# Kernel tuning notes

Measured on AMD Instinct MI355X. Metric: run time of the kernel, lower is better.

## Reference

```python
import jax, jax.numpy as jnp
import numpy as np

WINDOW = 128
LOOK_BACKWARD = 1
LOOK_FORWARD = 0  # causal=True -> look_forward defaults to 0
THETA = 10000.0


def look_around(x, backward=LOOK_BACKWARD, forward=LOOK_FORWARD, pad_value=-1):
    # x: (b, w, n, ...). Pad along window axis, concat shifted slices along token axis.
    w = x.shape[1]
    pad_width = [(0, 0)] * x.ndim
    pad_width[1] = (backward, forward)
    padded = jnp.pad(x, pad_width, constant_values=pad_value)
    return jnp.concatenate([padded[:, i:i + w] for i in range(forward + backward + 1)], axis=2)


def rotate_half(x):
    x1, x2 = jnp.split(x, 2, axis=-1)
    return jnp.concatenate((-x2, x1), axis=-1)


def setup_inputs() -> dict:
    key = jax.random.key(0)
    kq, kk, kv = jax.random.split(key, 3)
    shape = (32, 4096, 64)
    return {
        "q": jax.random.normal(kq, shape, dtype=jnp.float32),
        "k": jax.random.normal(kk, shape, dtype=jnp.float32),
        "v": jax.random.normal(kv, shape, dtype=jnp.float32),
    }


def reference(q, k, v):
    b, n, d = q.shape
    scale = d ** -0.5
    w = n // WINDOW

    bq = q.reshape(b, w, WINDOW, d) * scale
    bk = look_around(k.reshape(b, w, WINDOW, d), pad_value=-1.0)
    bv = look_around(v.reshape(b, w, WINDOW, d), pad_value=-1.0)
    j = bk.shape[2]  # (1 + look_backward + look_forward) * WINDOW = 256

    # rotary pos emb (SinusoidalEmbeddings, no xpos -> scale = 1)
    inv_freq = 1.0 / (THETA ** (jnp.arange(0, d, 2, dtype=jnp.float32) / d))
    t = jnp.arange(j, dtype=jnp.float32)
    freqs = jnp.einsum('i,j->ij', t, inv_freq)
    freqs = jnp.concatenate((freqs, freqs), axis=-1)  # (j, d)
    q_freqs = freqs[-WINDOW:]  # queries align to the last WINDOW positions
    bq = bq * jnp.cos(q_freqs) + rotate_half(bq) * jnp.sin(q_freqs)
    bk = bk * jnp.cos(freqs) + rotate_half(bk) * jnp.sin(freqs)

    # position bookkeeping for masks
    seq = jnp.arange(n)
    b_t = seq.reshape(1, w, WINDOW)           # (1, w, i)
    bq_t = b_t[..., :, None]                  # (1, w, i, 1)
    bq_k = look_around(b_t, pad_value=-1)[..., None, :]  # (1, w, 1, j)
    pad_mask = bq_k == -1
    causal_mask = bq_t < bq_k

    sim = jnp.einsum('bwie,bwje->bwij', bq, bk)  # (b, w, i, j)
    mask_value = -jnp.finfo(sim.dtype).max
    sim = jnp.where(causal_mask | pad_mask, mask_value, sim)

    attn = jax.nn.softmax(sim, axis=-1)
    out = jnp.einsum('bwij,bwje->bwie', attn, bv)
    return out.reshape(b, n, d)
```

## Files before the change

kernel.cpp:

```cpp
#include <hip/hip_runtime.h>
#include <hip/hip_bf16.h>

#define BDIM 512

typedef __attribute__((ext_vector_type(8))) _Float16 f16x8;
typedef __attribute__((ext_vector_type(4))) _Float16 f16x4;
typedef __attribute__((ext_vector_type(4))) float f32x4;

__global__ __launch_bounds__(512, 4)
void la_kernel(const float* __restrict__ qg, const float* __restrict__ kg,
               const float* __restrict__ vg, float* __restrict__ outg)
{
    __shared__ _Float16 Ks[128][72];
    __shared__ _Float16 Vt[64][140];

    const int ww = blockIdx.x, bb = blockIdx.y;
    const int tid = threadIdx.x;
    const size_t qbase = ((size_t)bb * 4096 + (size_t)ww * 128) * 64;
    const int srow0 = ww * 128 - 128;
    const float NEG = -3.0e38f;
    const float NLT32 = -0.28782313662425572f;

    const int wv = tid >> 6, lane = tid & 63, g = lane >> 4, c = lane & 15;
    const int qrow = wv * 16 + c;

    f16x8 qa0, qa1;
    {
        const float* p = qg + qbase + (size_t)qrow * 64 + 8 * g;
        float4 a0 = *(const float4*)p;
        float4 a1 = *(const float4*)(p + 4);
        float4 b0 = *(const float4*)(p + 32);
        float4 b1 = *(const float4*)(p + 36);
        float ra[8] = {a0.x,a0.y,a0.z,a0.w,a1.x,a1.y,a1.z,a1.w};
        float rb[8] = {b0.x,b0.y,b0.z,b0.w,b1.x,b1.y,b1.z,b1.w};
        float tq = (float)(128 + qrow);
        #pragma unroll
        for (int u = 0; u < 8; ++u) {
            float invf = __expf((float)(8 * g + u) * NLT32);
            float sn, cs; __sincosf(tq * invf, &sn, &cs);
            float a = ra[u] * 0.125f, b = rb[u] * 0.125f;
            qa0[u] = (_Float16)(a * cs - b * sn);
            qa1[u] = (_Float16)(b * cs + a * sn);
        }
    }

    f32x4 accO[4];
    #pragma unroll
    for (int nt = 0; nt < 4; ++nt) accO[nt] = (f32x4){0.f,0.f,0.f,0.f};
    float m = NEG, s = 0.f;

    #pragma unroll 1
    for (int h = 0; h < 2; ++h) {
        if (h == 0 && ww == 0) continue;
        if (h == 1) __syncthreads();

        #pragma unroll
        for (int it = 0; it < 2; ++it) {
            int task = tid + it * 512;
            int j = task >> 3, cb = (task & 7) << 2;
            int tj = 128 * h + j;
            const float* p = kg + ((size_t)bb * 4096 + srow0 + tj) * 64 + cb;
            float4 x1 = *(const float4*)p;
            float4 x2 = *(const float4*)(p + 32);
            const float* x1p = &x1.x;
            const float* x2p = &x2.x;
            f16x4 lo, hi;
            #pragma unroll
            for (int u = 0; u < 4; ++u) {
                float invf = __expf((float)(cb + u) * NLT32);
                float sn, cs; __sincosf((float)tj * invf, &sn, &cs);
                lo[u] = (_Float16)(x1p[u] * cs - x2p[u] * sn);
                hi[u] = (_Float16)(x2p[u] * cs + x1p[u] * sn);
            }
            *(f16x4*)&Ks[j][cb]      = lo;
            *(f16x4*)&Ks[j][cb + 32] = hi;
        }

        {
            int jq = tid >> 4, eq = tid & 15;
            int colb = ((jq & 24) << 2) + 8 * (jq & 3) + 4 * ((jq >> 2) & 1);
            float4 x[4];
            #pragma unroll
            for (int w = 0; w < 4; ++w)
                x[w] = *(const float4*)(vg + ((size_t)bb * 4096 + srow0 + 128 * h + 4 * jq + w) * 64 + 4 * eq);
            #pragma unroll
            for (int u = 0; u < 4; ++u) {
                f16x4 o;
                o[0] = (_Float16)((const float*)&x[0])[u];
                o[1] = (_Float16)((const float*)&x[1])[u];
                o[2] = (_Float16)((const float*)&x[2])[u];
                o[3] = (_Float16)((const float*)&x[3])[u];
                *(f16x4*)&Vt[4 * eq + u][colb] = o;
            }
        }

        __syncthreads();

        #pragma unroll
        for (int ch = 0; ch < 2; ++ch) {
            f32x4 acc[4];
            #pragma unroll
            for (int jt = 0; jt < 4; ++jt) acc[jt] = (f32x4){0.f,0.f,0.f,0.f};

            #pragma unroll
            for (int jt = 0; jt < 4; ++jt) {
                int row = ch * 64 + jt * 16 + c;
                f16x8 kb0 = *(const f16x8*)&Ks[row][8 * g];
                f16x8 kb1 = *(const f16x8*)&Ks[row][32 + 8 * g];
                acc[jt] = __builtin_amdgcn_mfma_f32_16x16x32_f16(kb0, qa0, acc[jt], 0, 0, 0);
                acc[jt] = __builtin_amdgcn_mfma_f32_16x16x32_f16(kb1, qa1, acc[jt], 0, 0, 0);
            }

            if (h == 1) {
                #pragma unroll
                for (int jt = 0; jt < 4; ++jt)
                    #pragma unroll
                    for (int r = 0; r < 4; ++r) {
                        int jj = ch * 64 + jt * 16 + 4 * g + r;
                        if (jj > qrow) acc[jt][r] = NEG;
                    }
            }

            float mx = NEG;
            #pragma unroll
            for (int jt = 0; jt < 4; ++jt)
                #pragma unroll
                for (int r = 0; r < 4; ++r) mx = fmaxf(mx, acc[jt][r]);
            mx = fmaxf(mx, __shfl_xor(mx, 16));
            mx = fmaxf(mx, __shfl_xor(mx, 32));

            float mnew = fmaxf(m, mx);
            float alpha = __expf(m - mnew);

            float ps = 0.f;
            f16x8 pa[2];
            #pragma unroll
            for (int jt = 0; jt < 4; ++jt)
                #pragma unroll
                for (int r = 0; r < 4; ++r) {
                    float p = __expf(acc[jt][r] - mnew);
                    ps += p;
                    pa[jt >> 1][(jt & 1) * 4 + r] = (_Float16)p;
                }
            ps += __shfl_xor(ps, 16);
            ps += __shfl_xor(ps, 32);

            s = s * alpha + ps;
            m = mnew;

            float alphaD[4];
            #pragma unroll
            for (int r = 0; r < 4; ++r)
                alphaD[r] = __shfl(alpha, (lane & 48) | (4 * g + r));
            #pragma unroll
            for (int nt = 0; nt < 4; ++nt)
                #pragma unroll
                for (int r = 0; r < 4; ++r) accO[nt][r] *= alphaD[r];

            #pragma unroll
            for (int st = 0; st < 2; ++st) {
                #pragma unroll
                for (int nt = 0; nt < 4; ++nt) {
                    f16x8 vb = *(const f16x8*)&Vt[nt * 16 + c][ch * 64 + st * 32 + 8 * g];
                    accO[nt] = __builtin_amdgcn_mfma_f32_16x16x32_f16(pa[st], vb, accO[nt], 0, 0, 0);
                }
            }
        }
    }

    float rcp = 1.0f / s;
    float rcpD[4];
    #pragma unroll
    for (int r = 0; r < 4; ++r)
        rcpD[r] = __shfl(rcp, (lane & 48) | (4 * g + r));

    float* op = outg + qbase + (size_t)(wv * 16) * 64;
    #pragma unroll
    for (int nt = 0; nt < 4; ++nt)
        #pragma unroll
        for (int r = 0; r < 4; ++r)
            op[(size_t)(4 * g + r) * 64 + nt * 16 + c] = accO[nt][r] * rcpD[r];
}

extern "C" void kernel_launch(void* const* d_in, const int* in_sizes, int n_in,
                              void* d_out, int out_size, void* d_ws, size_t ws_size,
                              hipStream_t stream) {
    (void)in_sizes; (void)n_in; (void)out_size; (void)d_ws; (void)ws_size;
    const float* q = (const float*)d_in[0];
    const float* k = (const float*)d_in[1];
    const float* v = (const float*)d_in[2];
    float* out = (float*)d_out;
    dim3 grid(32, 32);
    la_kernel<<<grid, BDIM, 0, stream>>>(q, k, v, out);
}
```

Before: 37.47 us.

## Process two windows per block, reusing shared K/V tile across windows

Each block now handles two adjacent query windows and keeps a two-slot shared buffer for K/V blocks, so the middle key/value block is loaded, rotary-encoded and converted once instead of twice. Rotary inverse frequencies are also precomputed once per thread rather than per element. This cuts global K/V traffic and rotary math by about a quarter. The cost is twice the shared memory, half as many blocks (fewer waves to hide latency), and serialized window processing inside a block.

```diff
diff --git a/kernel.cpp b/kernel.cpp
--- a/kernel.cpp
+++ b/kernel.cpp
@@ -11,55 +11,34 @@
 void la_kernel(const float* __restrict__ qg, const float* __restrict__ kg,
                const float* __restrict__ vg, float* __restrict__ outg)
 {
-    __shared__ _Float16 Ks[128][72];
-    __shared__ _Float16 Vt[64][140];
-
-    const int ww = blockIdx.x, bb = blockIdx.y;
+    __shared__ _Float16 Ks[2][128][72];
+    __shared__ _Float16 Vt[2][64][140];
+
+    const int wp = blockIdx.x, bb = blockIdx.y;
     const int tid = threadIdx.x;
-    const size_t qbase = ((size_t)bb * 4096 + (size_t)ww * 128) * 64;
-    const int srow0 = ww * 128 - 128;
+    const int wv = tid >> 6, lane = tid & 63, g = lane >> 4, c = lane & 15;
+    const int base = 256 * wp - 128;
     const float NEG = -3.0e38f;
     const float NLT32 = -0.28782313662425572f;
 
-    const int wv = tid >> 6, lane = tid & 63, g = lane >> 4, c = lane & 15;
-    const int qrow = wv * 16 + c;
-
-    f16x8 qa0, qa1;
-    {
-        const float* p = qg + qbase + (size_t)qrow * 64 + 8 * g;
-        float4 a0 = *(const float4*)p;
-        float4 a1 = *(const float4*)(p + 4);
-        float4 b0 = *(const float4*)(p + 32);
-        float4 b1 = *(const float4*)(p + 36);
-        float ra[8] = {a0.x,a0.y,a0.z,a0.w,a1.x,a1.y,a1.z,a1.w};
-        float rb[8] = {b0.x,b0.y,b0.z,b0.w,b1.x,b1.y,b1.z,b1.w};
-        float tq = (float)(128 + qrow);
-        #pragma unroll
-        for (int u = 0; u < 8; ++u) {
-            float invf = __expf((float)(8 * g + u) * NLT32);
-            float sn, cs; __sincosf(tq * invf, &sn, &cs);
-            float a = ra[u] * 0.125f, b = rb[u] * 0.125f;
-            qa0[u] = (_Float16)(a * cs - b * sn);
-            qa1[u] = (_Float16)(b * cs + a * sn);
-        }
-    }
-
-    f32x4 accO[4];
+    const int cbK = (tid & 7) << 2;
+    float invfK[4];
     #pragma unroll
-    for (int nt = 0; nt < 4; ++nt) accO[nt] = (f32x4){0.f,0.f,0.f,0.f};
-    float m = NEG, s = 0.f;
-
-    #pragma unroll 1
-    for (int h = 0; h < 2; ++h) {
-        if (h == 0 && ww == 0) continue;
-        if (h == 1) __syncthreads();
-
+    for (int u = 0; u < 4; ++u) invfK[u] = __expf((float)(cbK + u) * NLT32);
+    float invfQ[8];
+    #pragma unroll
+    for (int u = 0; u < 8; ++u) invfQ[u] = __expf((float)(8 * g + u) * NLT32);
+
+    const int jqV = tid >> 4, eqV = tid & 15;
+    const int colbV = ((jqV & 24) << 2) + 8 * (jqV & 3) + 4 * ((jqV >> 2) & 1);
+
+    auto stage = [&](int mm) {
+        int sl = mm & 1;
         #pragma unroll
         for (int it = 0; it < 2; ++it) {
-            int task = tid + it * 512;
-            int j = task >> 3, cb = (task & 7) << 2;
-            int tj = 128 * h + j;
-            const float* p = kg + ((size_t)bb * 4096 + srow0 + tj) * 64 + cb;
+            int j = (tid + it * 512) >> 3;
+            int t = 128 * mm + j;
+            const float* p = kg + ((size_t)bb * 4096 + base + t) * 64 + cbK;
             float4 x1 = *(const float4*)p;
             float4 x2 = *(const float4*)(p + 32);
             const float* x1p = &x1.x;
@@ -67,119 +46,155 @@
             f16x4 lo, hi;
             #pragma unroll
             for (int u = 0; u < 4; ++u) {
-                float invf = __expf((float)(cb + u) * NLT32);
-                float sn, cs; __sincosf((float)tj * invf, &sn, &cs);
+                float sn, cs; __sincosf((float)t * invfK[u], &sn, &cs);
                 lo[u] = (_Float16)(x1p[u] * cs - x2p[u] * sn);
                 hi[u] = (_Float16)(x2p[u] * cs + x1p[u] * sn);
             }
-            *(f16x4*)&Ks[j][cb]      = lo;
-            *(f16x4*)&Ks[j][cb + 32] = hi;
-        }
-
+            *(f16x4*)&Ks[sl][j][cbK]      = lo;
+            *(f16x4*)&Ks[sl][j][cbK + 32] = hi;
+        }
+        float4 x[4];
+        #pragma unroll
+        for (int w = 0; w < 4; ++w)
+            x[w] = *(const float4*)(vg + ((size_t)bb * 4096 + base + 128 * mm + 4 * jqV + w) * 64 + 4 * eqV);
+        #pragma unroll
+        for (int u = 0; u < 4; ++u) {
+            f16x4 o;
+            o[0] = (_Float16)((const float*)&x[0])[u];
+            o[1] = (_Float16)((const float*)&x[1])[u];
+            o[2] = (_Float16)((const float*)&x[2])[u];
+            o[3] = (_Float16)((const float*)&x[3])[u];
+            *(f16x4*)&Vt[sl][4 * eqV + u][colbV] = o;
+        }
+    };
+
+    auto computeWin = [&](int wi) {
+        const int qrow = tid < 0 ? 0 : (wv * 16 + c);
+        const int tq = 128 * (wi + 1) + qrow;
+
+        f16x8 qa0, qa1;
         {
-            int jq = tid >> 4, eq = tid & 15;
-            int colb = ((jq & 24) << 2) + 8 * (jq & 3) + 4 * ((jq >> 2) & 1);
-            float4 x[4];
-            #pragma unroll
-            for (int w = 0; w < 4; ++w)
-                x[w] = *(const float4*)(vg + ((size_t)bb * 4096 + srow0 + 128 * h + 4 * jq + w) * 64 + 4 * eq);
-            #pragma unroll
-            for (int u = 0; u < 4; ++u) {
-                f16x4 o;
-                o[0] = (_Float16)((const float*)&x[0])[u];
-                o[1] = (_Float16)((const float*)&x[1])[u];
-                o[2] = (_Float16)((const float*)&x[2])[u];
-                o[3] = (_Float16)((const float*)&x[3])[u];
-                *(f16x4*)&Vt[4 * eq + u][colb] = o;
+            const float* p = qg + ((size_t)bb * 4096 + base + tq) * 64 + 8 * g;
+            float4 a0 = *(const float4*)p;
+            float4 a1 = *(const float4*)(p + 4);
+            float4 b0 = *(const float4*)(p + 32);
+            float4 b1 = *(const float4*)(p + 36);
+            float ra[8] = {a0.x,a0.y,a0.z,a0.w,a1.x,a1.y,a1.z,a1.w};
+            float rb[8] = {b0.x,b0.y,b0.z,b0.w,b1.x,b1.y,b1.z,b1.w};
+            #pragma unroll
+            for (int u = 0; u < 8; ++u) {
+                float sn, cs; __sincosf((float)tq * invfQ[u], &sn, &cs);
+                float a = ra[u] * 0.125f, b = rb[u] * 0.125f;
+                qa0[u] = (_Float16)(a * cs - b * sn);
+                qa1[u] = (_Float16)(b * cs + a * sn);
             }
         }
 
-        __syncthreads();
-
-        #pragma unroll
-        for (int ch = 0; ch < 2; ++ch) {
-            f32x4 acc[4];
-            #pragma unroll
-            for (int jt = 0; jt < 4; ++jt) acc[jt] = (f32x4){0.f,0.f,0.f,0.f};
-
-            #pragma unroll
-            for (int jt = 0; jt < 4; ++jt) {
-                int row = ch * 64 + jt * 16 + c;
-                f16x8 kb0 = *(const f16x8*)&Ks[row][8 * g];
-                f16x8 kb1 = *(const f16x8*)&Ks[row][32 + 8 * g];
-                acc[jt] = __builtin_amdgcn_mfma_f32_16x16x32_f16(kb0, qa0, acc[jt], 0, 0, 0);
-                acc[jt] = __builtin_amdgcn_mfma_f32_16x16x32_f16(kb1, qa1, acc[jt], 0, 0, 0);
-            }
-
-            if (h == 1) {
+        f32x4 accO[4];
+        #pragma unroll
+        for (int nt = 0; nt < 4; ++nt) accO[nt] = (f32x4){0.f,0.f,0.f,0.f};
+        float m = NEG, s = 0.f;
+
+        #pragma unroll 1
+        for (int mm = wi; mm <= wi + 1; ++mm) {
+            if (wp == 0 && mm == 0) continue;
+            const int sl = mm & 1;
+            const bool causal = (mm == wi + 1);
+
+            #pragma unroll
+            for (int ch = 0; ch < 2; ++ch) {
+                f32x4 acc[4];
+                #pragma unroll
+                for (int jt = 0; jt < 4; ++jt) acc[jt] = (f32x4){0.f,0.f,0.f,0.f};
+
+                #pragma unroll
+                for (int jt = 0; jt < 4; ++jt) {
+                    int row = ch * 64 + jt * 16 + c;
+                    f16x8 kb0 = *(const f16x8*)&Ks[sl][row][8 * g];
+                    f16x8 kb1 = *(const f16x8*)&Ks[sl][row][32 + 8 * g];
+                    acc[jt] = __builtin_amdgcn_mfma_f32_16x16x32_f16(kb0, qa0, acc[jt], 0, 0, 0);
+                    acc[jt] = __builtin_amdgcn_mfma_f32_16x16x32_f16(kb1, qa1, acc[jt], 0, 0, 0);
+                }
+
+                if (causal) {
+                    #pragma unroll
+                    for (int jt = 0; jt < 4; ++jt)
+                        #pragma unroll
+                        for (int r = 0; r < 4; ++r) {
+                            int jj = ch * 64 + jt * 16 + 4 * g + r;
+                            if (jj > qrow) acc[jt][r] = NEG;
+                        }
+                }
+
+                float mx = NEG;
                 #pragma unroll
                 for (int jt = 0; jt < 4; ++jt)
                     #pragma unroll
+                    for (int r = 0; r < 4; ++r) mx = fmaxf(mx, acc[jt][r]);
+                mx = fmaxf(mx, __shfl_xor(mx, 16));
+                mx = fmaxf(mx, __shfl_xor(mx, 32));
+
+                float mnew = fmaxf(m, mx);
+                float alpha = __expf(m - mnew);
+
+                float ps = 0.f;
+                f16x8 pa[2];
+                #pragma unroll
+                for (int jt = 0; jt < 4; ++jt)
+                    #pragma unroll
                     for (int r = 0; r < 4; ++r) {
-                        int jj = ch * 64 + jt * 16 + 4 * g + r;
-                        if (jj > qrow) acc[jt][r] = NEG;
+                        float p = __expf(acc[jt][r] - mnew);
+                        ps += p;
+                        pa[jt >> 1][(jt & 1) * 4 + r] = (_Float16)p;
                     }
-            }
-
-            float mx = NEG;
-            #pragma unroll
-            for (int jt = 0; jt < 4; ++jt)
-                #pragma unroll
-                for (int r = 0; r < 4; ++r) mx = fmaxf(mx, acc[jt][r]);
-            mx = fmaxf(mx, __shfl_xor(mx, 16));
-            mx = fmaxf(mx, __shfl_xor(mx, 32));
-
-            float mnew = fmaxf(m, mx);
-            float alpha = __expf(m - mnew);
-
-            float ps = 0.f;
-            f16x8 pa[2];
-            #pragma unroll
-            for (int jt = 0; jt < 4; ++jt)
-                #pragma unroll
-                for (int r = 0; r < 4; ++r) {
-                    float p = __expf(acc[jt][r] - mnew);
-                    ps += p;
-                    pa[jt >> 1][(jt & 1) * 4 + r] = (_Float16)p;
-                }
-            ps += __shfl_xor(ps, 16);
-            ps += __shfl_xor(ps, 32);
-
-            s = s * alpha + ps;
-            m = mnew;
-
-            float alphaD[4];
-            #pragma unroll
-            for (int r = 0; r < 4; ++r)
-                alphaD[r] = __shfl(alpha, (lane & 48) | (4 * g + r));
-            #pragma unroll
-            for (int nt = 0; nt < 4; ++nt)
-                #pragma unroll
-                for (int r = 0; r < 4; ++r) accO[nt][r] *= alphaD[r];
-
-            #pragma unroll
-            for (int st = 0; st < 2; ++st) {
-                #pragma unroll
-                for (int nt = 0; nt < 4; ++nt) {
-                    f16x8 vb = *(const f16x8*)&Vt[nt * 16 + c][ch * 64 + st * 32 + 8 * g];
-                    accO[nt] = __builtin_amdgcn_mfma_f32_16x16x32_f16(pa[st], vb, accO[nt], 0, 0, 0);
+                ps += __shfl_xor(ps, 16);
+                ps += __shfl_xor(ps, 32);
+
+                s = s * alpha + ps;
+                m = mnew;
+
+                float alphaD[4];
+                #pragma unroll
+                for (int r = 0; r < 4; ++r)
+                    alphaD[r] = __shfl(alpha, (lane & 48) | (4 * g + r));
+                #pragma unroll
+                for (int nt = 0; nt < 4; ++nt)
+                    #pragma unroll
+                    for (int r = 0; r < 4; ++r) accO[nt][r] *= alphaD[r];
+
+                #pragma unroll
+                for (int st = 0; st < 2; ++st) {
+                    #pragma unroll
+                    for (int nt = 0; nt < 4; ++nt) {
+                        f16x8 vb = *(const f16x8*)&Vt[sl][nt * 16 + c][ch * 64 + st * 32 + 8 * g];
+                        accO[nt] = __builtin_amdgcn_mfma_f32_16x16x32_f16(pa[st], vb, accO[nt], 0, 0, 0);
+                    }
                 }
             }
         }
-    }
-
-    float rcp = 1.0f / s;
-    float rcpD[4];
-    #pragma unroll
-    for (int r = 0; r < 4; ++r)
-        rcpD[r] = __shfl(rcp, (lane & 48) | (4 * g + r));
-
-    float* op = outg + qbase + (size_t)(wv * 16) * 64;
-    #pragma unroll
-    for (int nt = 0; nt < 4; ++nt)
+
+        float rcp = 1.0f / s;
+        float rcpD[4];
         #pragma unroll
         for (int r = 0; r < 4; ++r)
-            op[(size_t)(4 * g + r) * 64 + nt * 16 + c] = accO[nt][r] * rcpD[r];
+            rcpD[r] = __shfl(rcp, (lane & 48) | (4 * g + r));
+
+        float* op = outg + ((size_t)bb * 4096 + base + 128 * (wi + 1) + wv * 16) * 64;
+        #pragma unroll
+        for (int nt = 0; nt < 4; ++nt)
+            #pragma unroll
+            for (int r = 0; r < 4; ++r)
+                op[(size_t)(4 * g + r) * 64 + nt * 16 + c] = accO[nt][r] * rcpD[r];
+    };
+
+    if (wp > 0) stage(0);
+    stage(1);
+    __syncthreads();
+    computeWin(0);
+    __syncthreads();
+    stage(2);
+    __syncthreads();
+    computeWin(1);
 }
 
 extern "C" void kernel_launch(void* const* d_in, const int* in_sizes, int n_in,
@@ -190,6 +205,6 @@
     const float* k = (const float*)d_in[1];
     const float* v = (const float*)d_in[2];
     float* out = (float*)d_out;
-    dim3 grid(32, 32);
+    dim3 grid(16, 32);
     la_kernel<<<grid, BDIM, 0, stream>>>(q, k, v, out);
 }
```

Result: faster. 34.00 us (-9.3%).

## Halve block size, give each wave two query tiles, skip fully masked chunks

Applied to the files above, without the earlier changes.

The block shrinks from 8 to 4 waves, and each wave now processes two 16-row query tiles, so every K/V fragment read from LDS feeds twice as many MFMAs. Inverse frequencies are hoisted out of the rotary loops. For the diagonal window, key chunks that are entirely above the causal diagonal for a query tile are skipped. The trade-off is higher register pressure from doubled accumulators and fewer threads to load and rotate K/V into shared memory.

```diff
diff --git a/kernel.cpp b/kernel.cpp
--- a/kernel.cpp
+++ b/kernel.cpp
@@ -1,13 +1,13 @@
 #include <hip/hip_runtime.h>
 #include <hip/hip_bf16.h>
 
-#define BDIM 512
+#define BDIM 256
 
 typedef __attribute__((ext_vector_type(8))) _Float16 f16x8;
 typedef __attribute__((ext_vector_type(4))) _Float16 f16x4;
 typedef __attribute__((ext_vector_type(4))) float f32x4;
 
-__global__ __launch_bounds__(512, 4)
+__global__ __launch_bounds__(256, 4)
 void la_kernel(const float* __restrict__ qg, const float* __restrict__ kg,
                const float* __restrict__ vg, float* __restrict__ outg)
 {
@@ -16,50 +16,60 @@
 
     const int ww = blockIdx.x, bb = blockIdx.y;
     const int tid = threadIdx.x;
-    const size_t qbase = ((size_t)bb * 4096 + (size_t)ww * 128) * 64;
+    const int wv = tid >> 6, lane = tid & 63, g = lane >> 4, c = lane & 15;
+    const size_t rowb = (size_t)bb * 4096;
     const int srow0 = ww * 128 - 128;
     const float NEG = -3.0e38f;
     const float NLT32 = -0.28782313662425572f;
 
-    const int wv = tid >> 6, lane = tid & 63, g = lane >> 4, c = lane & 15;
-    const int qrow = wv * 16 + c;
-
-    f16x8 qa0, qa1;
+    const int cbK = (tid & 7) << 2;
+    float invfK[4];
+    #pragma unroll
+    for (int u = 0; u < 4; ++u) invfK[u] = __expf((float)(cbK + u) * NLT32);
+
+    f16x8 qa0[2], qa1[2];
     {
-        const float* p = qg + qbase + (size_t)qrow * 64 + 8 * g;
-        float4 a0 = *(const float4*)p;
-        float4 a1 = *(const float4*)(p + 4);
-        float4 b0 = *(const float4*)(p + 32);
-        float4 b1 = *(const float4*)(p + 36);
-        float ra[8] = {a0.x,a0.y,a0.z,a0.w,a1.x,a1.y,a1.z,a1.w};
-        float rb[8] = {b0.x,b0.y,b0.z,b0.w,b1.x,b1.y,b1.z,b1.w};
-        float tq = (float)(128 + qrow);
-        #pragma unroll
-        for (int u = 0; u < 8; ++u) {
-            float invf = __expf((float)(8 * g + u) * NLT32);
-            float sn, cs; __sincosf(tq * invf, &sn, &cs);
-            float a = ra[u] * 0.125f, b = rb[u] * 0.125f;
-            qa0[u] = (_Float16)(a * cs - b * sn);
-            qa1[u] = (_Float16)(b * cs + a * sn);
+        float invfQ[8];
+        #pragma unroll
+        for (int u = 0; u < 8; ++u) invfQ[u] = __expf((float)(8 * g + u) * NLT32);
+        #pragma unroll
+        for (int mt = 0; mt < 2; ++mt) {
+            const int qrow = wv * 32 + mt * 16 + c;
+            const float* p = qg + (rowb + ww * 128 + qrow) * 64 + 8 * g;
+            float4 a0 = *(const float4*)p;
+            float4 a1 = *(const float4*)(p + 4);
+            float4 b0 = *(const float4*)(p + 32);
+            float4 b1 = *(const float4*)(p + 36);
+            float ra[8] = {a0.x,a0.y,a0.z,a0.w,a1.x,a1.y,a1.z,a1.w};
+            float rb[8] = {b0.x,b0.y,b0.z,b0.w,b1.x,b1.y,b1.z,b1.w};
+            float tq = (float)(128 + qrow);
+            #pragma unroll
+            for (int u = 0; u < 8; ++u) {
+                float sn, cs; __sincosf(tq * invfQ[u], &sn, &cs);
+                float a = ra[u] * 0.125f, b = rb[u] * 0.125f;
+                qa0[mt][u] = (_Float16)(a * cs - b * sn);
+                qa1[mt][u] = (_Float16)(b * cs + a * sn);
+            }
         }
     }
 
-    f32x4 accO[4];
+    f32x4 accO[2][4];
     #pragma unroll
-    for (int nt = 0; nt < 4; ++nt) accO[nt] = (f32x4){0.f,0.f,0.f,0.f};
-    float m = NEG, s = 0.f;
+    for (int mt = 0; mt < 2; ++mt)
+        #pragma unroll
+        for (int nt = 0; nt < 4; ++nt) accO[mt][nt] = (f32x4){0.f,0.f,0.f,0.f};
+    float m[2] = {NEG, NEG}, s[2] = {0.f, 0.f};
 
     #pragma unroll 1
     for (int h = 0; h < 2; ++h) {
         if (h == 0 && ww == 0) continue;
-        if (h == 1) __syncthreads();
-
-        #pragma unroll
-        for (int it = 0; it < 2; ++it) {
-            int task = tid + it * 512;
-            int j = task >> 3, cb = (task & 7) << 2;
-            int tj = 128 * h + j;
-            const float* p = kg + ((size_t)bb * 4096 + srow0 + tj) * 64 + cb;
+        if (h == 1 && ww != 0) __syncthreads();
+
+        #pragma unroll
+        for (int it = 0; it < 4; ++it) {
+            int j = (tid + it * 256) >> 3;
+            int t = 128 * h + j;
+            const float* p = kg + (rowb + srow0 + t) * 64 + cbK;
             float4 x1 = *(const float4*)p;
             float4 x2 = *(const float4*)(p + 32);
             const float* x1p = &x1.x;
@@ -67,22 +77,23 @@
             f16x4 lo, hi;
             #pragma unroll
             for (int u = 0; u < 4; ++u) {
-                float invf = __expf((float)(cb + u) * NLT32);
-                float sn, cs; __sincosf((float)tj * invf, &sn, &cs);
+                float sn, cs; __sincosf((float)t * invfK[u], &sn, &cs);
                 lo[u] = (_Float16)(x1p[u] * cs - x2p[u] * sn);
                 hi[u] = (_Float16)(x2p[u] * cs + x1p[u] * sn);
             }
-            *(f16x4*)&Ks[j][cb]      = lo;
-            *(f16x4*)&Ks[j][cb + 32] = hi;
-        }
-
-        {
-            int jq = tid >> 4, eq = tid & 15;
+            *(f16x4*)&Ks[j][cbK]      = lo;
+            *(f16x4*)&Ks[j][cbK + 32] = hi;
+        }
+
+        #pragma unroll
+        for (int it = 0; it < 2; ++it) {
+            int task = tid + it * 256;
+            int jq = task >> 4, eq = task & 15;
             int colb = ((jq & 24) << 2) + 8 * (jq & 3) + 4 * ((jq >> 2) & 1);
             float4 x[4];
             #pragma unroll
             for (int w = 0; w < 4; ++w)
-                x[w] = *(const float4*)(vg + ((size_t)bb * 4096 + srow0 + 128 * h + 4 * jq + w) * 64 + 4 * eq);
+                x[w] = *(const float4*)(vg + (rowb + srow0 + 128 * h + 4 * jq + w) * 64 + 4 * eq);
             #pragma unroll
             for (int u = 0; u < 4; ++u) {
                 f16x4 o;
@@ -97,89 +108,98 @@
         __syncthreads();
 
         #pragma unroll
-        for (int ch = 0; ch < 2; ++ch) {
-            f32x4 acc[4];
-            #pragma unroll
-            for (int jt = 0; jt < 4; ++jt) acc[jt] = (f32x4){0.f,0.f,0.f,0.f};
-
-            #pragma unroll
-            for (int jt = 0; jt < 4; ++jt) {
-                int row = ch * 64 + jt * 16 + c;
-                f16x8 kb0 = *(const f16x8*)&Ks[row][8 * g];
-                f16x8 kb1 = *(const f16x8*)&Ks[row][32 + 8 * g];
-                acc[jt] = __builtin_amdgcn_mfma_f32_16x16x32_f16(kb0, qa0, acc[jt], 0, 0, 0);
-                acc[jt] = __builtin_amdgcn_mfma_f32_16x16x32_f16(kb1, qa1, acc[jt], 0, 0, 0);
-            }
-
-            if (h == 1) {
+        for (int mt = 0; mt < 2; ++mt) {
+            const int qrow = wv * 32 + mt * 16 + c;
+            #pragma unroll
+            for (int ch = 0; ch < 2; ++ch) {
+                if (h == 1 && ch == 1 && (wv * 32 + mt * 16) <= 48) continue;
+
+                f32x4 acc[4];
+                #pragma unroll
+                for (int jt = 0; jt < 4; ++jt) acc[jt] = (f32x4){0.f,0.f,0.f,0.f};
+
+                #pragma unroll
+                for (int jt = 0; jt < 4; ++jt) {
+                    int row = ch * 64 + jt * 16 + c;
+                    f16x8 kb0 = *(const f16x8*)&Ks[row][8 * g];
+                    f16x8 kb1 = *(const f16x8*)&Ks[row][32 + 8 * g];
+                    acc[jt] = __builtin_amdgcn_mfma_f32_16x16x32_f16(kb0, qa0[mt], acc[jt], 0, 0, 0);
+                    acc[jt] = __builtin_amdgcn_mfma_f32_16x16x32_f16(kb1, qa1[mt], acc[jt], 0, 0, 0);
+                }
+
+                if (h == 1) {
+                    #pragma unroll
+                    for (int jt = 0; jt < 4; ++jt)
+                        #pragma unroll
+                        for (int r = 0; r < 4; ++r) {
+                            int jj = ch * 64 + jt * 16 + 4 * g + r;
+                            if (jj > qrow) acc[jt][r] = NEG;
+                        }
+                }
+
+                float mx = NEG;
                 #pragma unroll
                 for (int jt = 0; jt < 4; ++jt)
                     #pragma unroll
+                    for (int r = 0; r < 4; ++r) mx = fmaxf(mx, acc[jt][r]);
+                mx = fmaxf(mx, __shfl_xor(mx, 16));
+                mx = fmaxf(mx, __shfl_xor(mx, 32));
+
+                float mnew = fmaxf(m[mt], mx);
+                float alpha = __expf(m[mt] - mnew);
+
+                float ps = 0.f;
+                f16x8 pa[2];
+                #pragma unroll
+                for (int jt = 0; jt < 4; ++jt)
+                    #pragma unroll
                     for (int r = 0; r < 4; ++r) {
-                        int jj = ch * 64 + jt * 16 + 4 * g + r;
-                        if (jj > qrow) acc[jt][r] = NEG;
+                        float p = __expf(acc[jt][r] - mnew);
+                        ps += p;
+                        pa[jt >> 1][(jt & 1) * 4 + r] = (_Float16)p;
                     }
-            }
-
-            float mx = NEG;
-            #pragma unroll
-            for (int jt = 0; jt < 4; ++jt)
-                #pragma unroll
-                for (int r = 0; r < 4; ++r) mx = fmaxf(mx, acc[jt][r]);
-            mx = fmaxf(mx, __shfl_xor(mx, 16));
-            mx = fmaxf(mx, __shfl_xor(mx, 32));
-
-            float mnew = fmaxf(m, mx);
-            float alpha = __expf(m - mnew);
-
-            float ps = 0.f;
-            f16x8 pa[2];
-            #pragma unroll
-            for (int jt = 0; jt < 4; ++jt)
-                #pragma unroll
-                for (int r = 0; r < 4; ++r) {
-                    float p = __expf(acc[jt][r] - mnew);
-                    ps += p;
-                    pa[jt >> 1][(jt & 1) * 4 + r] = (_Float16)p;
+                ps += __shfl_xor(ps, 16);
+                ps += __shfl_xor(ps, 32);
+
+                s[mt] = s[mt] * alpha + ps;
+                m[mt] = mnew;
+
+                float alphaD[4];
+                #pragma unroll
+                for (int r = 0; r < 4; ++r)
+                    alphaD[r] = __shfl(alpha, (lane & 48) | (4 * g + r));
+                #pragma unroll
+                for (int nt = 0; nt < 4; ++nt)
+                    #pragma unroll
+                    for (int r = 0; r < 4; ++r) accO[mt][nt][r] *= alphaD[r];
+
+                #pragma unroll
+                for (int st = 0; st < 2; ++st) {
+                    #pragma unroll
+                    for (int nt = 0; nt < 4; ++nt) {
+                        f16x8 vb = *(const f16x8*)&Vt[nt * 16 + c][ch * 64 + st * 32 + 8 * g];
+                        accO[mt][nt] = __builtin_amdgcn_mfma_f32_16x16x32_f16(pa[st], vb, accO[mt][nt], 0, 0, 0);
+                    }
                 }
-            ps += __shfl_xor(ps, 16);
-            ps += __shfl_xor(ps, 32);
-
-            s = s * alpha + ps;
-            m = mnew;
-
-            float alphaD[4];
+            }
+        }
+    }
+
+    #pragma unroll
+    for (int mt = 0; mt < 2; ++mt) {
+        float rcp = 1.0f / s[mt];
+        float rcpD[4];
+        #pragma unroll
+        for (int r = 0; r < 4; ++r)
+            rcpD[r] = __shfl(rcp, (lane & 48) | (4 * g + r));
+
+        float* op = outg + (rowb + ww * 128 + wv * 32 + mt * 16) * 64;
+        #pragma unroll
+        for (int nt = 0; nt < 4; ++nt)
             #pragma unroll
             for (int r = 0; r < 4; ++r)
-                alphaD[r] = __shfl(alpha, (lane & 48) | (4 * g + r));
-            #pragma unroll
-            for (int nt = 0; nt < 4; ++nt)
-                #pragma unroll
-                for (int r = 0; r < 4; ++r) accO[nt][r] *= alphaD[r];
-
-            #pragma unroll
-            for (int st = 0; st < 2; ++st) {
-                #pragma unroll
-                for (int nt = 0; nt < 4; ++nt) {
-                    f16x8 vb = *(const f16x8*)&Vt[nt * 16 + c][ch * 64 + st * 32 + 8 * g];
-                    accO[nt] = __builtin_amdgcn_mfma_f32_16x16x32_f16(pa[st], vb, accO[nt], 0, 0, 0);
-                }
-            }
-        }
+                op[(size_t)(4 * g + r) * 64 + nt * 16 + c] = accO[mt][nt][r] * rcpD[r];
     }
-
-    float rcp = 1.0f / s;
-    float rcpD[4];
-    #pragma unroll
-    for (int r = 0; r < 4; ++r)
-        rcpD[r] = __shfl(rcp, (lane & 48) | (4 * g + r));
-
-    float* op = outg + qbase + (size_t)(wv * 16) * 64;
-    #pragma unroll
-    for (int nt = 0; nt < 4; ++nt)
-        #pragma unroll
-        for (int r = 0; r < 4; ++r)
-            op[(size_t)(4 * g + r) * 64 + nt * 16 + c] = accO[nt][r] * rcpD[r];
 }
 
 extern "C" void kernel_launch(void* const* d_in, const int* in_sizes, int n_in,
```

Result: slower. 38.68 us (+3.2%).
